# Performance work log

Hardware: AMD Instinct MI355X
Metric: run time of the kernel (lower is better)

## Reference

```python
import jax, jax.numpy as jnp
import numpy as np

B, T, D = 8, 2048, 1024
H, C, DV = 8, 64, 128   # n_heads, latent_dim, d_head
LN_EPS = 1e-5
NORM_EPS = 1e-12  # F.normalize eps


def _xavier(k, shape, fan_in, fan_out):
    lim = float(np.sqrt(6.0 / (fan_in + fan_out)))
    return jax.random.uniform(k, shape, jnp.float32, -lim, lim)


def setup_inputs() -> dict:
    key = jax.random.key(0)
    ks = jax.random.split(key, 9)
    x = jax.random.normal(ks[0], (B, T, D), jnp.float32)
    Wq = _xavier(ks[1], (C, D), D, C)            # S_q weight (out,in)
    Wk = _xavier(ks[2], (C, D), D, C)            # S_k
    Wv = _xavier(ks[3], (C, D), D, C)            # S_v
    Qc = _xavier(ks[4], (H, C, C), C, C)         # per-head latent rotations
    Vc = _xavier(ks[5], (H, C, DV), C, DV)       # per-head value up-proj
    Wa_w = _xavier(ks[6], (H * C, D), D, H * C)  # W_alpha weight
    Wa_b = jnp.full((H * C,), 3.0, jnp.float32)  # W_alpha bias init = 3.0
    Wo = _xavier(ks[7], (D, H * DV), H * DV, D)  # output proj
    gamma = jnp.ones((D,), jnp.float32)
    beta = jnp.zeros((D,), jnp.float32)
    return {"x": x, "Wq": Wq, "Wk": Wk, "Wv": Wv, "Qc": Qc, "Vc": Vc,
            "Wa_w": Wa_w, "Wa_b": Wa_b, "Wo": Wo, "gamma": gamma, "beta": beta}


def _forward(x, Wq, Wk, Wv, Qc, Vc, Wa_w, Wa_b, Wo, gamma, beta):
    residual = x
    # LayerNorm (biased variance, like torch)
    mu = jnp.mean(x, axis=-1, keepdims=True)
    var = jnp.mean(jnp.square(x - mu), axis=-1, keepdims=True)
    xn = (x - mu) * jax.lax.rsqrt(var + LN_EPS) * gamma + beta

    q_lat = xn @ Wq.T          # (B,T,C)
    k_lat = xn @ Wk.T          # (B,T,C) shared across heads
    v_lat = xn @ Wv.T          # (B,T,C)

    q = jnp.einsum('btc,hce->bhte', q_lat, Qc)   # (B,H,T,C)
    v = jnp.einsum('btc,hcd->bhtd', v_lat, Vc)   # (B,H,T,DV)
    alpha = jax.nn.sigmoid(xn @ Wa_w.T + Wa_b)   # (B,T,H*C)
    alpha = alpha.reshape(x.shape[0], x.shape[1], H, C).transpose(0, 2, 1, 3)  # (B,H,T,C)

    # F.normalize(k, dim=-1): k / max(||k||, eps)
    kn = k_lat / jnp.maximum(jnp.linalg.norm(k_lat, axis=-1, keepdims=True), NORM_EPS)

    # time-major for scan
    qs = jnp.moveaxis(q, 2, 0)      # (T,B,H,C)
    vs = jnp.moveaxis(v, 2, 0)      # (T,B,H,DV)
    als = jnp.moveaxis(alpha, 2, 0)  # (T,B,H,C)
    kns = jnp.moveaxis(kn, 1, 0)    # (T,B,C)

    S0 = jnp.zeros((x.shape[0], H, C, DV), x.dtype)

    def step(S, inp):
        q_t, k_t, v_t, a_t = inp
        # S_t = diag(alpha_t) S_{t-1} + k_t v_t^T  (k shared across heads)
        S = a_t[..., None] * S + k_t[:, None, :, None] * v_t[..., None, :]
        o_t = jnp.einsum('bhcv,bhc->bhv', S, q_t)
        return S, o_t

    _, outs = jax.lax.scan(step, S0, (qs, kns, vs, als))  # outs: (T,B,H,DV)
    out = jnp.moveaxis(outs, 0, 1).reshape(x.shape[0], x.shape[1], H * DV)
    return out @ Wo.T + residual


def reference(x, Wq, Wk, Wv, Qc, Vc, Wa_w, Wa_b, Wo, gamma, beta):
    return _forward(x, Wq, Wk, Wv, Qc, Vc, Wa_w, Wa_b, Wo, gamma, beta)
```

## Files before the change

kernel.cpp:

```cpp
#include <hip/hip_runtime.h>

typedef unsigned short u16;
typedef unsigned int   u32;
typedef __bf16 bf16x8 __attribute__((ext_vector_type(8)));
typedef float  f32x4  __attribute__((ext_vector_type(4)));
typedef float  f32x8  __attribute__((ext_vector_type(8)));

#define B_  8
#define T_  2048
#define D_  1024
#define H_  8
#define C_  64
#define DV_ 128
#define M_  (B_*T_)
#define L_  128
#define NC_ (T_/L_)

__device__ __forceinline__ u16 f2bf(float f){
  u32 u = __float_as_uint(f);
  u32 r = (u + 0x7fffu + ((u >> 16) & 1u)) >> 16;
  return (u16)r;
}
__device__ __forceinline__ float bf2f(u16 u){
  return __uint_as_float(((u32)u) << 16);
}

__global__ __launch_bounds__(256) void ln_kernel(
    const float* __restrict__ x, const float* __restrict__ gamma,
    const float* __restrict__ beta, u16* __restrict__ xnb){
  const int m = blockIdx.x;
  const int tid = threadIdx.x;
  const int wave = tid >> 6, lane = tid & 63;
  const float* xr = x + (size_t)m * D_;
  float4 xv = *(const float4*)&xr[tid*4];
  float s = xv.x + xv.y + xv.z + xv.w;
  #pragma unroll
  for (int off = 32; off > 0; off >>= 1) s += __shfl_xor(s, off, 64);
  __shared__ float red[8];
  if (lane == 0) red[wave] = s;
  __syncthreads();
  float mu = (red[0]+red[1]+red[2]+red[3]) * (1.f/1024.f);
  float dx = xv.x-mu, dy = xv.y-mu, dz = xv.z-mu, dw = xv.w-mu;
  float ss = dx*dx + dy*dy + dz*dz + dw*dw;
  #pragma unroll
  for (int off = 32; off > 0; off >>= 1) ss += __shfl_xor(ss, off, 64);
  if (lane == 0) red[4+wave] = ss;
  __syncthreads();
  float var = (red[4]+red[5]+red[6]+red[7]) * (1.f/1024.f);
  float rs = rsqrtf(var + 1e-5f);
  float4 g  = *(const float4*)&gamma[tid*4];
  float4 bb = *(const float4*)&beta[tid*4];
  ushort4 o4;
  o4.x = f2bf(dx*rs*g.x + bb.x);
  o4.y = f2bf(dy*rs*g.y + bb.y);
  o4.z = f2bf(dz*rs*g.z + bb.z);
  o4.w = f2bf(dw*rs*g.w + bb.w);
  *(ushort4*)&xnb[(size_t)m*D_ + tid*4] = o4;
}

__global__ __launch_bounds__(256) void prep_weights(
    const float* __restrict__ Wq, const float* __restrict__ Wk,
    const float* __restrict__ Wv, const float* __restrict__ Wa,
    const float* __restrict__ Qc, const float* __restrict__ Vc,
    const float* __restrict__ Wo,
    u16* __restrict__ Wcatb, u16* __restrict__ QcTb,
    u16* __restrict__ VcTb,  u16* __restrict__ Wob){
  int idx = blockIdx.x * 256 + threadIdx.x;
  if (idx < 720896){
    int r = idx >> 10, col = idx & 1023;
    float v;
    if (r < 64)       v = Wq[(size_t)r*1024 + col];
    else if (r < 128) v = Wk[(size_t)(r-64)*1024 + col];
    else if (r < 192) v = Wv[(size_t)(r-128)*1024 + col];
    else              v = Wa[(size_t)(r-192)*1024 + col];
    Wcatb[idx] = f2bf(v);
  } else if (idx < 753664){
    int i = idx - 720896;
    int n = i >> 6, c = i & 63; int h = n >> 6, e = n & 63;
    QcTb[i] = f2bf(Qc[((size_t)h*64 + c)*64 + e]);
  } else if (idx < 819200){
    int i = idx - 753664;
    int n = i >> 6, c = i & 63; int h = n >> 7, d = n & 127;
    VcTb[i] = f2bf(Vc[((size_t)h*64 + c)*128 + d]);
  } else if (idx < 1867776){
    int i = idx - 819200;
    Wob[i] = f2bf(Wo[i]);
  }
}

__global__ __launch_bounds__(256) void gemm_bf16(
    const u16* __restrict__ A, const u16* __restrict__ Bw,
    float* __restrict__ C, const float* __restrict__ res,
    u16* __restrict__ Cb, int N, int K){
  __shared__ u16 As[128][36];
  __shared__ u16 Bs[64][36];
  const int tid = threadIdx.x;
  const int wave = tid >> 6;
  const int lane = tid & 63;
  const int q  = lane >> 4;
  const int mr = lane & 15;
  const int m0 = blockIdx.x * 128;
  const int n0 = blockIdx.y * 64;

  union FragU { u32 u[4]; bf16x8 v; };
  f32x4 zero = {0.f, 0.f, 0.f, 0.f};
  f32x4 acc[2][4];
  #pragma unroll
  for (int i = 0; i < 2; i++)
    #pragma unroll
    for (int j = 0; j < 4; j++) acc[i][j] = zero;

  for (int k0 = 0; k0 < K; k0 += 32){
    #pragma unroll
    for (int p = 0; p < 2; ++p){
      int ch = p*256 + tid;
      int r = ch >> 2, c4 = ch & 3;
      const uint4 val = *(const uint4*)(&A[(size_t)(m0 + r)*K + k0 + c4*8]);
      u32* dst = (u32*)&As[r][c4*8];
      dst[0]=val.x; dst[1]=val.y; dst[2]=val.z; dst[3]=val.w;
    }
    {
      int r = tid >> 2, c4 = tid & 3;
      const uint4 val = *(const uint4*)(&Bw[(size_t)(n0 + r)*K + k0 + c4*8]);
      u32* dst = (u32*)&Bs[r][c4*8];
      dst[0]=val.x; dst[1]=val.y; dst[2]=val.z; dst[3]=val.w;
    }
    __syncthreads();
    bf16x8 afr[2], bfr[4];
    #pragma unroll
    for (int mt = 0; mt < 2; mt++){
      const u32* p = (const u32*)&As[wave*32 + mt*16 + mr][q*8];
      FragU f; f.u[0]=p[0]; f.u[1]=p[1]; f.u[2]=p[2]; f.u[3]=p[3];
      afr[mt] = f.v;
    }
    #pragma unroll
    for (int nt = 0; nt < 4; nt++){
      const u32* p = (const u32*)&Bs[nt*16 + mr][q*8];
      FragU f; f.u[0]=p[0]; f.u[1]=p[1]; f.u[2]=p[2]; f.u[3]=p[3];
      bfr[nt] = f.v;
    }
    #pragma unroll
    for (int mt = 0; mt < 2; mt++)
      #pragma unroll
      for (int nt = 0; nt < 4; nt++)
        acc[mt][nt] = __builtin_amdgcn_mfma_f32_16x16x32_bf16(
            afr[mt], bfr[nt], acc[mt][nt], 0, 0, 0);
    __syncthreads();
  }

  #pragma unroll
  for (int mt = 0; mt < 2; mt++)
    #pragma unroll
    for (int nt = 0; nt < 4; nt++)
      #pragma unroll
      for (int r = 0; r < 4; r++){
        int row = m0 + wave*32 + mt*16 + q*4 + r;
        int col = n0 + nt*16 + mr;
        size_t idx = (size_t)row * N + col;
        float v = acc[mt][nt][r];
        if (res) v += res[idx];
        if (Cb) Cb[idx] = f2bf(v);
        else    C[idx] = v;
      }
}

__global__ __launch_bounds__(256) void split_proj(
    const float* __restrict__ proj, const float* __restrict__ Wab,
    u16* __restrict__ qlatb, float* __restrict__ knf,
    u16* __restrict__ vlatb, float* __restrict__ alphaf){
  const int m = blockIdx.x * 4 + (threadIdx.x >> 6);
  const int lane = threadIdx.x & 63;
  const float* pr = proj + (size_t)m * 704;
  qlatb[(size_t)m*64 + lane] = f2bf(pr[lane]);
  float kv = pr[64 + lane];
  float ss = kv * kv;
  #pragma unroll
  for (int off = 32; off > 0; off >>= 1) ss += __shfl_xor(ss, off, 64);
  float nrm = fmaxf(sqrtf(ss), 1e-12f);
  knf[(size_t)m*64 + lane] = kv / nrm;
  vlatb[(size_t)m*64 + lane] = f2bf(pr[128 + lane]);
  #pragma unroll
  for (int j = 0; j < 8; j++){
    int jj = j*64 + lane;
    float av = pr[192 + jj] + Wab[jj];
    alphaf[(size_t)m*512 + jj] = 1.f / (1.f + expf(-av));
  }
}


__global__ __launch_bounds__(512, 8) void scan_pass1(
    const float* __restrict__ knf, const u16* __restrict__ vb,
    const float* __restrict__ alphaf,
    float* __restrict__ Sbuf, float* __restrict__ btot){
  const int ch = blockIdx.x;
  const int bh = blockIdx.y;
  const int b = bh >> 3, h = bh & 7;
  const int tid = threadIdx.x;
  const int w = __builtin_amdgcn_readfirstlane(tid >> 6);
  const int dg = tid & 63;
  const int t0 = ch * L_;

  const float* kp  = knf    + ((size_t)(b*T_ + t0))*64  + w*8;
  const float* ap  = alphaf + ((size_t)(b*T_ + t0))*512 + h*64 + w*8;
  const float* alp = ap + (dg & 7);
  const u32*   vp  = (const u32*)(vb + ((size_t)(b*T_ + t0))*1024 + h*128) + dg;

  float S[8][2];
  #pragma unroll
  for (int j = 0; j < 8; j++){ S[j][0] = 0.f; S[j][1] = 0.f; }
  float bt = 1.f;

  for (int t = 0; t < L_; t += 2){
    f32x8 a0, a1, k0, k1;
    asm volatile(
      "s_load_dwordx8 %0, %4, 0x0\n\t"
      "s_load_dwordx8 %1, %4, 0x800\n\t"
      "s_load_dwordx8 %2, %5, 0x0\n\t"
      "s_load_dwordx8 %3, %5, 0x100\n\t"
      "s_waitcnt lgkmcnt(0)"
      : "=&s"(a0), "=&s"(a1), "=&s"(k0), "=&s"(k1)
      : "s"(ap), "s"(kp));
    float al0 = alp[0], al1 = alp[512];
    u32 vv0 = vp[0], vv1 = vp[512];
    float v00 = __uint_as_float(vv0 << 16);
    float v01 = __uint_as_float(vv0 & 0xffff0000u);
    float v10 = __uint_as_float(vv1 << 16);
    float v11 = __uint_as_float(vv1 & 0xffff0000u);
    #pragma unroll
    for (int j = 0; j < 8; j++){
      S[j][0] = a0[j]*S[j][0] + k0[j]*v00;
      S[j][1] = a0[j]*S[j][1] + k0[j]*v01;
    }
    bt *= al0;
    #pragma unroll
    for (int j = 0; j < 8; j++){
      S[j][0] = a1[j]*S[j][0] + k1[j]*v10;
      S[j][1] = a1[j]*S[j][1] + k1[j]*v11;
    }
    bt *= al1;
    ap += 1024; kp += 128; alp += 1024; vp += 1024;
  }

  float* Sl = Sbuf + ((size_t)bh*NC_ + ch) * (64*128);
  #pragma unroll
  for (int j = 0; j < 8; j++)
    *(float2*)&Sl[(size_t)(w*8+j)*128 + 2*dg] = make_float2(S[j][0], S[j][1]);
  if (dg < 8) btot[((size_t)bh*NC_ + ch)*64 + w*8 + dg] = bt;
}

__global__ __launch_bounds__(256) void scan_combine(
    float* __restrict__ Sbuf, const float* __restrict__ btot){
  const int bh = blockIdx.x;
  const int tid = threadIdx.x;
  float S[32];
  #pragma unroll
  for (int i = 0; i < 32; i++) S[i] = 0.f;
  float*       Sb  = Sbuf + (size_t)bh*NC_*8192;
  const float* btb = btot + (size_t)bh*NC_*64;
  for (int j = 0; j < NC_; j++){
    if (j < NC_-1){
      #pragma unroll
      for (int i = 0; i < 32; i++){
        int e = i*256 + tid;
        float loc = Sb[(size_t)j*8192 + e];
        float bv  = btb[j*64 + (e >> 7)];
        Sb[(size_t)j*8192 + e] = S[i];
        S[i] = bv * S[i] + loc;
      }
    } else {
      #pragma unroll
      for (int i = 0; i < 32; i++) Sb[(size_t)j*8192 + i*256 + tid] = S[i];
    }
  }
}

__global__ __launch_bounds__(512, 8) void scan_pass2(
    const float* __restrict__ qf, const float* __restrict__ knf,
    const u16* __restrict__ vb, const float* __restrict__ alphaf,
    const float* __restrict__ Sbuf, u16* __restrict__ ob){
  const int ch = blockIdx.x;
  const int bh = blockIdx.y;
  const int b = bh >> 3, h = bh & 7;
  const int tid = threadIdx.x;
  const int w = __builtin_amdgcn_readfirstlane(tid >> 6);
  const int dg = tid & 63;
  const int t0 = ch * L_;
  __shared__ __align__(16) float sO[2][8][4][128];

  const float* qp = qf     + ((size_t)(b*T_ + t0))*512 + h*64 + w*8;
  const float* kp = knf    + ((size_t)(b*T_ + t0))*64  + w*8;
  const float* ap = alphaf + ((size_t)(b*T_ + t0))*512 + h*64 + w*8;
  const u32*   vp = (const u32*)(vb + ((size_t)(b*T_ + t0))*1024 + h*128) + dg;
  u16* obase = ob + ((size_t)(b*T_ + t0))*1024 + h*128;

  float S[8][2];
  const float* Si = Sbuf + ((size_t)bh*NC_ + ch) * (64*128);
  #pragma unroll
  for (int j = 0; j < 8; j++){
    float2 s2 = *(const float2*)&Si[(size_t)(w*8+j)*128 + 2*dg];
    S[j][0] = s2.x; S[j][1] = s2.y;
  }

  const int rtt = tid >> 7, rdd = tid & 127;

  for (int sb = 0; sb < L_/4; sb++){
    const int p = sb & 1;
    #pragma unroll
    for (int half = 0; half < 2; half++){
      f32x8 a0, a1, k0, k1, q0, q1;
      asm volatile(
        "s_load_dwordx8 %0, %6, 0x0\n\t"
        "s_load_dwordx8 %1, %6, 0x800\n\t"
        "s_load_dwordx8 %2, %7, 0x0\n\t"
        "s_load_dwordx8 %3, %7, 0x100\n\t"
        "s_load_dwordx8 %4, %8, 0x0\n\t"
        "s_load_dwordx8 %5, %8, 0x800\n\t"
        "s_waitcnt lgkmcnt(0)"
        : "=&s"(a0), "=&s"(a1), "=&s"(k0), "=&s"(k1), "=&s"(q0), "=&s"(q1)
        : "s"(ap), "s"(kp), "s"(qp));
      u32 vv0 = vp[0], vv1 = vp[512];
      float v00 = __uint_as_float(vv0 << 16);
      float v01 = __uint_as_float(vv0 & 0xffff0000u);
      float v10 = __uint_as_float(vv1 << 16);
      float v11 = __uint_as_float(vv1 & 0xffff0000u);
      {
        float oa0, oa1, ob0, ob1;
        S[0][0] = a0[0]*S[0][0] + k0[0]*v00;  oa0 = S[0][0]*q0[0];
        S[0][1] = a0[0]*S[0][1] + k0[0]*v01;  oa1 = S[0][1]*q0[0];
        S[1][0] = a0[1]*S[1][0] + k0[1]*v00;  ob0 = S[1][0]*q0[1];
        S[1][1] = a0[1]*S[1][1] + k0[1]*v01;  ob1 = S[1][1]*q0[1];
        #pragma unroll
        for (int j = 2; j < 8; j += 2){
          S[j][0]   = a0[j]*S[j][0]     + k0[j]*v00;    oa0 += S[j][0]*q0[j];
          S[j][1]   = a0[j]*S[j][1]     + k0[j]*v01;    oa1 += S[j][1]*q0[j];
          S[j+1][0] = a0[j+1]*S[j+1][0] + k0[j+1]*v00;  ob0 += S[j+1][0]*q0[j+1];
          S[j+1][1] = a0[j+1]*S[j+1][1] + k0[j+1]*v01;  ob1 += S[j+1][1]*q0[j+1];
        }
        *(float2*)&sO[p][w][half*2+0][2*dg] = make_float2(oa0+ob0, oa1+ob1);
      }
      {
        float oa0, oa1, ob0, ob1;
        S[0][0] = a1[0]*S[0][0] + k1[0]*v10;  oa0 = S[0][0]*q1[0];
        S[0][1] = a1[0]*S[0][1] + k1[0]*v11;  oa1 = S[0][1]*q1[0];
        S[1][0] = a1[1]*S[1][0] + k1[1]*v10;  ob0 = S[1][0]*q1[1];
        S[1][1] = a1[1]*S[1][1] + k1[1]*v11;  ob1 = S[1][1]*q1[1];
        #pragma unroll
        for (int j = 2; j < 8; j += 2){
          S[j][0]   = a1[j]*S[j][0]     + k1[j]*v10;    oa0 += S[j][0]*q1[j];
          S[j][1]   = a1[j]*S[j][1]     + k1[j]*v11;    oa1 += S[j][1]*q1[j];
          S[j+1][0] = a1[j+1]*S[j+1][0] + k1[j+1]*v10;  ob0 += S[j+1][0]*q1[j+1];
          S[j+1][1] = a1[j+1]*S[j+1][1] + k1[j+1]*v11;  ob1 += S[j+1][1]*q1[j+1];
        }
        *(float2*)&sO[p][w][half*2+1][2*dg] = make_float2(oa0+ob0, oa1+ob1);
      }
      ap += 1024; kp += 128; qp += 1024; vp += 1024;
    }
    __syncthreads();
    float o = sO[p][0][rtt][rdd] + sO[p][1][rtt][rdd]
            + sO[p][2][rtt][rdd] + sO[p][3][rtt][rdd]
            + sO[p][4][rtt][rdd] + sO[p][5][rtt][rdd]
            + sO[p][6][rtt][rdd] + sO[p][7][rtt][rdd];
    obase[(size_t)(sb*4 + rtt)*1024 + rdd] = f2bf(o);
  }
}

extern "C" void kernel_launch(void* const* d_in, const int* in_sizes, int n_in,
                              void* d_out, int out_size, void* d_ws, size_t ws_size,
                              hipStream_t stream){
  const float* x     = (const float*)d_in[0];
  const float* Wq    = (const float*)d_in[1];
  const float* Wk    = (const float*)d_in[2];
  const float* Wv    = (const float*)d_in[3];
  const float* Qc    = (const float*)d_in[4];
  const float* Vc    = (const float*)d_in[5];
  const float* Wa_w  = (const float*)d_in[6];
  const float* Wa_b  = (const float*)d_in[7];
  const float* Wo    = (const float*)d_in[8];
  const float* gamma = (const float*)d_in[9];
  const float* beta  = (const float*)d_in[10];
  float* out = (float*)d_out;

  char* ws = (char*)d_ws;
  size_t off = 0;
  auto alloc = [&](size_t bytes) -> void* {
    void* p = ws + off; off += (bytes + 255) & ~(size_t)255; return p;
  };
  char* R1 = (char*)alloc((size_t)M_ * 1024 * 2);
  u16*   xnb  = (u16*)R1;
  u16*   obuf = (u16*)R1;
  char* R2 = (char*)alloc((size_t)M_ * 704 * 4);
  float* proj = (float*)R2;
  float* qf   = (float*)R2;
  float* Sbuf   = (float*)alloc((size_t)64 * NC_ * 8192 * 4);
  u16*   vfb    = (u16*)alloc((size_t)M_ * 1024 * 2);
  float* alphaf = (float*)alloc((size_t)M_ * 512 * 4);
  float* knf    = (float*)alloc((size_t)M_ * 64 * 4);
  u16*   qlatb  = (u16*)alloc((size_t)M_ * 64 * 2);
  u16*   vlatb  = (u16*)alloc((size_t)M_ * 64 * 2);
  u16*   Wcatb  = (u16*)alloc((size_t)704 * 1024 * 2);
  u16*   QcTb   = (u16*)alloc((size_t)512 * 64 * 2);
  u16*   VcTb   = (u16*)alloc((size_t)1024 * 64 * 2);
  u16*   Wob    = (u16*)alloc((size_t)1024 * 1024 * 2);
  float* btotp  = (float*)alloc((size_t)64 * NC_ * 64 * 4);
  (void)ws_size; (void)in_sizes; (void)n_in; (void)out_size;

  ln_kernel<<<dim3(M_), dim3(256), 0, stream>>>(x, gamma, beta, xnb);
  prep_weights<<<dim3(7296), dim3(256), 0, stream>>>(
      Wq, Wk, Wv, Wa_w, Qc, Vc, Wo, Wcatb, QcTb, VcTb, Wob);
  gemm_bf16<<<dim3(M_/128, 704/64), dim3(256), 0, stream>>>(
      xnb, Wcatb, proj, nullptr, nullptr, 704, 1024);
  split_proj<<<dim3(M_/4), dim3(256), 0, stream>>>(
      proj, Wa_b, qlatb, knf, vlatb, alphaf);
  gemm_bf16<<<dim3(M_/128, 1024/64), dim3(256), 0, stream>>>(
      vlatb, VcTb, nullptr, nullptr, vfb, 1024, 64);
  gemm_bf16<<<dim3(M_/128, 512/64), dim3(256), 0, stream>>>(
      qlatb, QcTb, qf, nullptr, nullptr, 512, 64);
  scan_pass1<<<dim3(NC_-1, 64), dim3(512), 0, stream>>>(
      knf, vfb, alphaf, Sbuf, btotp);
  scan_combine<<<dim3(64), dim3(256), 0, stream>>>(Sbuf, btotp);
  scan_pass2<<<dim3(NC_, 64), dim3(512), 0, stream>>>(
      qf, knf, vfb, alphaf, Sbuf, obuf);
  gemm_bf16<<<dim3(M_/128, 1024/64), dim3(256), 0, stream>>>(
      obuf, Wob, out, x, nullptr, 1024, 1024);
}
```

Measured before the change: 538.9 us.

## Enlarge GEMM tiles to 128x128 with direct global-to-LDS loads and parallelize scan combine

The bf16 GEMM moves from a 128x64 tile to a 128x128 tile arranged as a 2x2 wave grid. Tiles are staged with global_load_lds, which copies straight into LDS without passing through registers, and the padded LDS layout is dropped. Weight rows are padded to 768 so the projection GEMM divides evenly, and stores are guarded by column. scan_combine now spreads its elements across many more blocks, one thread per element, replacing 64 blocks that each looped over 32 elements. The aim is more data reuse per tile and more parallelism in the combine step; the unpadded LDS layout may add bank conflicts, and there is one sync per K step with no double buffering.

```diff
diff --git a/kernel.cpp b/kernel.cpp
--- a/kernel.cpp
+++ b/kernel.cpp
@@ -23,6 +23,12 @@
 }
 __device__ __forceinline__ float bf2f(u16 u){
   return __uint_as_float(((u32)u) << 16);
+}
+
+typedef const __attribute__((address_space(1))) unsigned int* gp1_t;
+typedef __attribute__((address_space(3))) unsigned int* lp3_t;
+__device__ __forceinline__ void stage16(const void* g, void* l){
+  __builtin_amdgcn_global_load_lds((gp1_t)g, (lp3_t)l, 16, 0, 0);
 }
 
 __global__ __launch_bounds__(256) void ln_kernel(
@@ -66,24 +72,24 @@
     u16* __restrict__ Wcatb, u16* __restrict__ QcTb,
     u16* __restrict__ VcTb,  u16* __restrict__ Wob){
   int idx = blockIdx.x * 256 + threadIdx.x;
-  if (idx < 720896){
+  if (idx < 786432){
     int r = idx >> 10, col = idx & 1023;
-    float v;
+    float v = 0.f;
     if (r < 64)       v = Wq[(size_t)r*1024 + col];
     else if (r < 128) v = Wk[(size_t)(r-64)*1024 + col];
     else if (r < 192) v = Wv[(size_t)(r-128)*1024 + col];
-    else              v = Wa[(size_t)(r-192)*1024 + col];
+    else if (r < 704) v = Wa[(size_t)(r-192)*1024 + col];
     Wcatb[idx] = f2bf(v);
-  } else if (idx < 753664){
-    int i = idx - 720896;
+  } else if (idx < 819200){
+    int i = idx - 786432;
     int n = i >> 6, c = i & 63; int h = n >> 6, e = n & 63;
     QcTb[i] = f2bf(Qc[((size_t)h*64 + c)*64 + e]);
-  } else if (idx < 819200){
-    int i = idx - 753664;
+  } else if (idx < 884736){
+    int i = idx - 819200;
     int n = i >> 6, c = i & 63; int h = n >> 7, d = n & 127;
     VcTb[i] = f2bf(Vc[((size_t)h*64 + c)*128 + d]);
-  } else if (idx < 1867776){
-    int i = idx - 819200;
+  } else {
+    int i = idx - 884736;
     Wob[i] = f2bf(Wo[i]);
   }
 }
@@ -92,55 +98,60 @@
     const u16* __restrict__ A, const u16* __restrict__ Bw,
     float* __restrict__ C, const float* __restrict__ res,
     u16* __restrict__ Cb, int N, int K){
-  __shared__ u16 As[128][36];
-  __shared__ u16 Bs[64][36];
+  __shared__ u16 As[128*32];
+  __shared__ u16 Bs[128*32];
   const int tid = threadIdx.x;
   const int wave = tid >> 6;
   const int lane = tid & 63;
   const int q  = lane >> 4;
   const int mr = lane & 15;
+  const int wr = wave >> 1, wc = wave & 1;
   const int m0 = blockIdx.x * 128;
-  const int n0 = blockIdx.y * 64;
-
-  union FragU { u32 u[4]; bf16x8 v; };
+  const int n0 = blockIdx.y * 128;
+
+  const int j0 = wave*2;
+  const int lr = lane >> 2;
+  const int lc = (lane & 3) * 8;
+  const u16* pa0 = A  + (size_t)(m0 + (j0  )*16 + lr)*K + lc;
+  const u16* pa1 = A  + (size_t)(m0 + (j0+1)*16 + lr)*K + lc;
+  const u16* pb0 = Bw + (size_t)(n0 + (j0  )*16 + lr)*K + lc;
+  const u16* pb1 = Bw + (size_t)(n0 + (j0+1)*16 + lr)*K + lc;
+  u16* la0 = &As[(j0  )*512];
+  u16* la1 = &As[(j0+1)*512];
+  u16* lb0 = &Bs[(j0  )*512];
+  u16* lb1 = &Bs[(j0+1)*512];
+
+  union FragU { uint4 u4; bf16x8 v; };
   f32x4 zero = {0.f, 0.f, 0.f, 0.f};
-  f32x4 acc[2][4];
-  #pragma unroll
-  for (int i = 0; i < 2; i++)
+  f32x4 acc[4][4];
+  #pragma unroll
+  for (int i = 0; i < 4; i++)
     #pragma unroll
     for (int j = 0; j < 4; j++) acc[i][j] = zero;
 
+  const u16* fA = &As[(size_t)(wr*64 + mr)*32 + q*8];
+  const u16* fB = &Bs[(size_t)(wc*64 + mr)*32 + q*8];
+
   for (int k0 = 0; k0 < K; k0 += 32){
-    #pragma unroll
-    for (int p = 0; p < 2; ++p){
-      int ch = p*256 + tid;
-      int r = ch >> 2, c4 = ch & 3;
-      const uint4 val = *(const uint4*)(&A[(size_t)(m0 + r)*K + k0 + c4*8]);
-      u32* dst = (u32*)&As[r][c4*8];
-      dst[0]=val.x; dst[1]=val.y; dst[2]=val.z; dst[3]=val.w;
-    }
-    {
-      int r = tid >> 2, c4 = tid & 3;
-      const uint4 val = *(const uint4*)(&Bw[(size_t)(n0 + r)*K + k0 + c4*8]);
-      u32* dst = (u32*)&Bs[r][c4*8];
-      dst[0]=val.x; dst[1]=val.y; dst[2]=val.z; dst[3]=val.w;
-    }
+    stage16(pa0, la0);
+    stage16(pa1, la1);
+    stage16(pb0, lb0);
+    stage16(pb1, lb1);
+    pa0 += 32; pa1 += 32; pb0 += 32; pb1 += 32;
     __syncthreads();
-    bf16x8 afr[2], bfr[4];
-    #pragma unroll
-    for (int mt = 0; mt < 2; mt++){
-      const u32* p = (const u32*)&As[wave*32 + mt*16 + mr][q*8];
-      FragU f; f.u[0]=p[0]; f.u[1]=p[1]; f.u[2]=p[2]; f.u[3]=p[3];
+    bf16x8 afr[4], bfr[4];
+    #pragma unroll
+    for (int mt = 0; mt < 4; mt++){
+      FragU f; f.u4 = *(const uint4*)(fA + mt*512);
       afr[mt] = f.v;
     }
     #pragma unroll
     for (int nt = 0; nt < 4; nt++){
-      const u32* p = (const u32*)&Bs[nt*16 + mr][q*8];
-      FragU f; f.u[0]=p[0]; f.u[1]=p[1]; f.u[2]=p[2]; f.u[3]=p[3];
+      FragU f; f.u4 = *(const uint4*)(fB + nt*512);
       bfr[nt] = f.v;
     }
     #pragma unroll
-    for (int mt = 0; mt < 2; mt++)
+    for (int mt = 0; mt < 4; mt++)
       #pragma unroll
       for (int nt = 0; nt < 4; nt++)
         acc[mt][nt] = __builtin_amdgcn_mfma_f32_16x16x32_bf16(
@@ -149,19 +160,22 @@
   }
 
   #pragma unroll
-  for (int mt = 0; mt < 2; mt++)
-    #pragma unroll
-    for (int nt = 0; nt < 4; nt++)
-      #pragma unroll
-      for (int r = 0; r < 4; r++){
-        int row = m0 + wave*32 + mt*16 + q*4 + r;
-        int col = n0 + nt*16 + mr;
-        size_t idx = (size_t)row * N + col;
-        float v = acc[mt][nt][r];
-        if (res) v += res[idx];
-        if (Cb) Cb[idx] = f2bf(v);
-        else    C[idx] = v;
+  for (int mt = 0; mt < 4; mt++)
+    #pragma unroll
+    for (int nt = 0; nt < 4; nt++){
+      int col = n0 + wc*64 + nt*16 + mr;
+      if (col < N){
+        #pragma unroll
+        for (int r = 0; r < 4; r++){
+          int row = m0 + wr*64 + mt*16 + q*4 + r;
+          size_t idx = (size_t)row * N + col;
+          float v = acc[mt][nt][r];
+          if (res) v += res[idx];
+          if (Cb) Cb[idx] = f2bf(v);
+          else    C[idx] = v;
+        }
       }
+    }
 }
 
 __global__ __launch_bounds__(256) void split_proj(
@@ -250,27 +264,16 @@
 
 __global__ __launch_bounds__(256) void scan_combine(
     float* __restrict__ Sbuf, const float* __restrict__ btot){
-  const int bh = blockIdx.x;
-  const int tid = threadIdx.x;
-  float S[32];
-  #pragma unroll
-  for (int i = 0; i < 32; i++) S[i] = 0.f;
-  float*       Sb  = Sbuf + (size_t)bh*NC_*8192;
-  const float* btb = btot + (size_t)bh*NC_*64;
+  const int bh = blockIdx.y;
+  const int e  = blockIdx.x * 256 + threadIdx.x;
+  float*       Sb  = Sbuf + (size_t)bh*NC_*8192 + e;
+  const float* btb = btot + (size_t)bh*NC_*64 + (e >> 7);
+  float S = 0.f;
+  #pragma unroll
   for (int j = 0; j < NC_; j++){
-    if (j < NC_-1){
-      #pragma unroll
-      for (int i = 0; i < 32; i++){
-        int e = i*256 + tid;
-        float loc = Sb[(size_t)j*8192 + e];
-        float bv  = btb[j*64 + (e >> 7)];
-        Sb[(size_t)j*8192 + e] = S[i];
-        S[i] = bv * S[i] + loc;
-      }
-    } else {
-      #pragma unroll
-      for (int i = 0; i < 32; i++) Sb[(size_t)j*8192 + i*256 + tid] = S[i];
-    }
+    float loc = Sb[(size_t)j*8192];
+    Sb[(size_t)j*8192] = S;
+    if (j < NC_-1) S = btb[j*64] * S + loc;
   }
 }
 
@@ -397,7 +400,7 @@
   float* knf    = (float*)alloc((size_t)M_ * 64 * 4);
   u16*   qlatb  = (u16*)alloc((size_t)M_ * 64 * 2);
   u16*   vlatb  = (u16*)alloc((size_t)M_ * 64 * 2);
-  u16*   Wcatb  = (u16*)alloc((size_t)704 * 1024 * 2);
+  u16*   Wcatb  = (u16*)alloc((size_t)768 * 1024 * 2);
   u16*   QcTb   = (u16*)alloc((size_t)512 * 64 * 2);
   u16*   VcTb   = (u16*)alloc((size_t)1024 * 64 * 2);
   u16*   Wob    = (u16*)alloc((size_t)1024 * 1024 * 2);
@@ -405,21 +408,21 @@
   (void)ws_size; (void)in_sizes; (void)n_in; (void)out_size;
 
   ln_kernel<<<dim3(M_), dim3(256), 0, stream>>>(x, gamma, beta, xnb);
-  prep_weights<<<dim3(7296), dim3(256), 0, stream>>>(
+  prep_weights<<<dim3(7552), dim3(256), 0, stream>>>(
       Wq, Wk, Wv, Wa_w, Qc, Vc, Wo, Wcatb, QcTb, VcTb, Wob);
-  gemm_bf16<<<dim3(M_/128, 704/64), dim3(256), 0, stream>>>(
+  gemm_bf16<<<dim3(M_/128, 6), dim3(256), 0, stream>>>(
       xnb, Wcatb, proj, nullptr, nullptr, 704, 1024);
   split_proj<<<dim3(M_/4), dim3(256), 0, stream>>>(
       proj, Wa_b, qlatb, knf, vlatb, alphaf);
-  gemm_bf16<<<dim3(M_/128, 1024/64), dim3(256), 0, stream>>>(
+  gemm_bf16<<<dim3(M_/128, 8), dim3(256), 0, stream>>>(
       vlatb, VcTb, nullptr, nullptr, vfb, 1024, 64);
-  gemm_bf16<<<dim3(M_/128, 512/64), dim3(256), 0, stream>>>(
+  gemm_bf16<<<dim3(M_/128, 4), dim3(256), 0, stream>>>(
       qlatb, QcTb, qf, nullptr, nullptr, 512, 64);
   scan_pass1<<<dim3(NC_-1, 64), dim3(512), 0, stream>>>(
       knf, vfb, alphaf, Sbuf, btotp);
-  scan_combine<<<dim3(64), dim3(256), 0, stream>>>(Sbuf, btotp);
+  scan_combine<<<dim3(32, 64), dim3(256), 0, stream>>>(Sbuf, btotp);
   scan_pass2<<<dim3(NC_, 64), dim3(512), 0, stream>>>(
       qf, knf, vfb, alphaf, Sbuf, obuf);
-  gemm_bf16<<<dim3(M_/128, 1024/64), dim3(256), 0, stream>>>(
+  gemm_bf16<<<dim3(M_/128, 8), dim3(256), 0, stream>>>(
       obuf, Wob, out, x, nullptr, 1024, 1024);
 }
```

Result: faster. 520.6 us (-3.4%).
